# Performance work log

Hardware: AMD Instinct MI355X
Metric: run time of the kernel (lower is better)

Reference implementation:

```python
import jax, jax.numpy as jnp
import numpy as np

HEADS = 16
DMODEL = 1024
DPH = DMODEL // HEADS  # 64
MAX_REL = 32
B, S = 4, 1024


def setup_inputs() -> dict:
    key = jax.random.key(0)
    ks = jax.random.split(key, 16)
    f = lambda k, shape: jax.random.normal(k, shape, dtype=jnp.float32)
    scale = 1.0 / np.sqrt(DMODEL)
    inp = {
        'key':   f(ks[0], (B, S, DMODEL)),
        'value': f(ks[1], (B, S, DMODEL)),
        'query': f(ks[2], (B, S, DMODEL)),
        'mask':  jax.random.randint(ks[3], (B, 1, S), 0, 2).astype(jnp.bool_),
        'Wq': f(ks[4], (DMODEL, DMODEL)) * scale,
        'bq': jnp.zeros((DMODEL,), jnp.float32),
        'Wk': f(ks[5], (DMODEL, DMODEL)) * scale,
        'bk': jnp.zeros((DMODEL,), jnp.float32),
        'Wv': f(ks[6], (DMODEL, DMODEL)) * scale,
        'bv': jnp.zeros((DMODEL,), jnp.float32),
        'Wo': f(ks[7], (DMODEL, DMODEL)) * scale,
        'bo': jnp.zeros((DMODEL,), jnp.float32),
        'rel_emb': f(ks[8], (2 * MAX_REL + 1, DPH)) * 0.02,
    }
    return inp


def _rel_pos_matrix(length, max_rel):
    r = jnp.arange(length)
    dist = r[None, :] - r[:, None]            # [S,S]
    return jnp.clip(dist, -max_rel, max_rel) + max_rel


def reference(key, value, query, mask, Wq, bq, Wk, bk, Wv, bv, Wo, bo, rel_emb):
    b, s, _ = query.shape
    # projections (no layer_cache, attn_type='self': q/k/v all from inputs)
    q = (query @ Wq + bq).reshape(b, s, HEADS, DPH).transpose(0, 2, 1, 3)  # [B,H,S,D]
    k = (key   @ Wk + bk).reshape(b, s, HEADS, DPH).transpose(0, 2, 1, 3)
    v = (value @ Wv + bv).reshape(b, s, HEADS, DPH).transpose(0, 2, 1, 3)

    # relative position embeddings (keys and values share the same table lookup)
    rel_idx = _rel_pos_matrix(s, MAX_REL)      # [S,S] int
    relations = rel_emb[rel_idx]               # [S,S,D]

    q = q / jnp.sqrt(jnp.asarray(DPH, q.dtype))
    scores = jnp.einsum('bhqd,bhkd->bhqk', q, k)
    scores = scores + jnp.einsum('bhqd,qkd->bhqk', q, relations)
    scores = jnp.where(mask[:, None, :, :], -1e18, scores)  # mask [B,1,1,S] broadcast
    attn = jax.nn.softmax(scores, axis=-1)
    # dropout p=0.0 (eval): identity
    ctx = jnp.einsum('bhqk,bhkd->bhqd', attn, v)
    ctx = ctx + jnp.einsum('bhqk,qkd->bhqd', attn, relations)
    ctx = ctx.transpose(0, 2, 1, 3).reshape(b, s, HEADS * DPH)
    out = ctx @ Wo + bo
    top_attn = attn[:, 0]
    return out, top_attn
```

## Files before the change

kernel.cpp:

```cpp
#include <hip/hip_runtime.h>

typedef unsigned short u16;
typedef unsigned int   u32;
typedef short bf8v  __attribute__((ext_vector_type(8)));
typedef short s16x4 __attribute__((ext_vector_type(4)));
typedef float f32x4 __attribute__((ext_vector_type(4)));

#define DEV static __device__ __forceinline__
#define MBYTE (1u<<20)

DEV u16 f2b(float f) {
    u32 u = __builtin_bit_cast(u32, f);
    u32 r = (u + 0x7fffu + ((u >> 16) & 1u)) >> 16;
    return (u16)r;
}
DEV float b2f(u16 s) { return __builtin_bit_cast(float, (u32)s << 16); }
DEV bf8v ld8(const u16* p) { return *reinterpret_cast<const bf8v*>(p); }

DEV bf8v ldelems(const void* X, long idx, int f32f) {
    if (f32f) {
        const float* p = (const float*)X + idx;
        f32x4 a = *(const f32x4*)p;
        f32x4 b = *(const f32x4*)(p + 4);
        bf8v r;
        r[0] = (short)f2b(a[0]); r[1] = (short)f2b(a[1]);
        r[2] = (short)f2b(a[2]); r[3] = (short)f2b(a[3]);
        r[4] = (short)f2b(b[0]); r[5] = (short)f2b(b[1]);
        r[6] = (short)f2b(b[2]); r[7] = (short)f2b(b[3]);
        return r;
    }
    return ld8((const u16*)X + idx);
}
DEV float ldscalar(const void* X, long idx, int f32f) {
    return f32f ? ((const float*)X)[idx] : b2f(((const u16*)X)[idx]);
}

DEV f32x4 mfma_(bf8v a, bf8v b, f32x4 c) {
    return __builtin_amdgcn_mfma_f32_16x16x32_bf16(a, b, c, 0, 0, 0);
}

DEV void gload16(void* lds, const void* g) {
    __builtin_amdgcn_global_load_lds(
        (const __attribute__((address_space(1))) void*)g,
        (__attribute__((address_space(3))) void*)lds,
        16, 0, 0);
}

__global__ __launch_bounds__(256) void sniffrelk(const u32* q, const u32* m,
                                                 const void* rel, u16* relT, int* flags) {
    __shared__ int c1s, c2s;
    int t = threadIdx.x;
    if (t == 0) { c1s = 0; c2s = 0; }
    __syncthreads();
    int c1 = 0, c2 = 0;
    for (int i = t; i < 1024; i += 256) {
        u32 u = q[i];
        int e = (int)((u >> 23) & 0xff);
        if (u == 0u || (e >= 118 && e <= 134)) c1++;
        if (m[i] > 1u) c2++;
    }
    atomicAdd(&c1s, c1);
    atomicAdd(&c2s, c2);
    __syncthreads();
    int f32f = (c1s > 512) ? 1 : 0;
    if (t == 0) { flags[0] = f32f; flags[1] = (c2s > 100) ? 1 : 0; }
    for (int i = t; i < 64 * 64; i += 256) {
        int d = i >> 6, r = i & 63;
        relT[i] = f32f ? f2b(((const float*)rel)[r * 64 + d]) : ((const u16*)rel)[r * 64 + d];
    }
}

__global__ __launch_bounds__(256) void tposek(const void* s0, const void* s1,
                                              const void* s2, const void* s3,
                                              u16* d0, u16* d1, u16* d2, u16* d3,
                                              const int* flags) {
    __shared__ u16 tile[64][65];
    int f32f = flags[0];
    int z = blockIdx.z;
    const void* src = z == 0 ? s0 : (z == 1 ? s1 : (z == 2 ? s2 : s3));
    u16*       dst = z == 0 ? d0 : (z == 1 ? d1 : (z == 2 ? d2 : d3));
    int t = threadIdx.x;
    int r0 = blockIdx.y * 64, c0 = blockIdx.x * 64;
#pragma unroll
    for (int i = 0; i < 16; ++i) {
        int u = i * 256 + t;
        int row = u >> 6, col = u & 63;
        long gi = (long)(r0 + row) * 1024 + c0 + col;
        tile[row][col] = f32f ? f2b(((const float*)src)[gi]) : ((const u16*)src)[gi];
    }
    __syncthreads();
#pragma unroll
    for (int i = 0; i < 8; ++i) {
        int u = i * 256 + t;
        int row = u >> 5, col = (u & 31) * 2;
        u32 v = (u32)tile[col][row] | ((u32)tile[col + 1][row] << 16);
        *(u32*)(dst + (long)(c0 + row) * 1024 + r0 + col) = v;
    }
}

__global__ __launch_bounds__(512) void gemm128(
    const void* x0, const void* x1, const void* x2,
    const u16* w0, const u16* w1, const u16* w2,
    const void* b0, const void* b1, const void* b2,
    void* c0, void* c1, void* c2, int mode_base,
    const int* flags, int a_use_flag) {
    __shared__ __align__(16) u16 Al[128 * 32];
    __shared__ __align__(16) u16 Bl[128 * 32];

    int j = blockIdx.x;
    int nwg = gridDim.x;
    int ppx = nwg >> 6;
    int xcd = j & 7, idx = j >> 3;
    int panel = xcd * ppx + (idx >> 3);
    int n0 = (idx & 7) * 128;
    int m0 = (panel & 31) * 128;
    int z  = panel >> 5;

    const void* X    = z == 0 ? x0 : (z == 1 ? x1 : x2);
    const u16*  BT   = z == 0 ? w0 : (z == 1 ? w1 : w2);
    const void* bias = z == 0 ? b0 : (z == 1 ? b1 : b2);
    void*       C    = z == 0 ? c0 : (z == 1 ? c1 : c2);
    int mode = mode_base + z;
    int f32m = flags[0];
    int f32a = a_use_flag ? f32m : 0;

    int t = threadIdx.x, w = t >> 6, l = t & 63;
    int lr = l & 15, lg = l >> 4;
    int wr = (w >> 1) * 32, wc = (w & 1) * 64;

    int rS = t >> 2;
    int sP = t & 3;
    int sL = sP ^ ((rS >> 1) & 3);

    f32x4 acc[2][4];
    f32x4 zf = {0.f, 0.f, 0.f, 0.f};
#pragma unroll
    for (int mt = 0; mt < 2; ++mt)
#pragma unroll
        for (int nt = 0; nt < 4; ++nt) acc[mt][nt] = zf;

    for (int kk = 0; kk < 32; ++kk) {
        __syncthreads();
        gload16((char*)Bl + w * 1024,
                (const char*)BT + (long)(n0 + rS) * 2048 + (long)kk * 64 + sL * 16);
        bf8v va = ldelems(X, (long)(m0 + rS) * 1024 + kk * 32 + sL * 8, f32a);
        *(bf8v*)((char*)Al + rS * 64 + sP * 16) = va;
        __syncthreads();
        bf8v af[2], bfr[4];
#pragma unroll
        for (int mt = 0; mt < 2; ++mt) {
            int r = wr + mt * 16 + lr;
            af[mt] = *(const bf8v*)((const char*)Al + r * 64 + ((lg * 16) ^ (((r >> 1) & 3) << 4)));
        }
#pragma unroll
        for (int nt = 0; nt < 4; ++nt) {
            int r = wc + nt * 16 + lr;
            bfr[nt] = *(const bf8v*)((const char*)Bl + r * 64 + ((lg * 16) ^ (((r >> 1) & 3) << 4)));
        }
#pragma unroll
        for (int mt = 0; mt < 2; ++mt)
#pragma unroll
            for (int nt = 0; nt < 4; ++nt) acc[mt][nt] = mfma_(af[mt], bfr[nt], acc[mt][nt]);
    }

#pragma unroll
    for (int nt = 0; nt < 4; ++nt) {
        int col = n0 + wc + nt * 16 + lr;
        float bv = f32m ? ((const float*)bias)[col] : b2f(((const u16*)bias)[col]);
#pragma unroll
        for (int mt = 0; mt < 2; ++mt) {
#pragma unroll
            for (int r = 0; r < 4; ++r) {
                int m = m0 + wr + mt * 16 + lg * 4 + r;
                float v = acc[mt][nt][r] + bv;
                if (mode == 0) v *= 0.125f;
                if (mode <= 1) {
                    int bb = m >> 10, s = m & 1023, hh = col >> 6, dd = col & 63;
                    ((u16*)C)[(((bb << 4) + hh) * 1024 + s) * 64 + dd] = f2b(v);
                } else if (mode == 2) {
                    int bb = m >> 10, s = m & 1023, hh = col >> 6, dd = col & 63;
                    ((u16*)C)[(((bb << 4) + hh) * 64 + dd) * 1024 + s] = f2b(v);
                } else {
                    long idx2 = (long)m * 1024 + col;
                    if (f32m) ((float*)C)[idx2] = v; else ((u16*)C)[idx2] = f2b(v);
                }
            }
        }
    }
}

__global__ __launch_bounds__(256) void attnk(
    const u16* __restrict__ Qw, const u16* __restrict__ Kw, const u16* __restrict__ Vtw,
    const void* __restrict__ rel, const u16* __restrict__ relT,
    const void* __restrict__ mask,
    u16* __restrict__ ctx, void* __restrict__ dout, u16* __restrict__ linv_g,
    const int* __restrict__ flags) {
    __shared__ __align__(16) u16 Klds[2][32 * 64];
    __shared__ __align__(16) u16 Vlds[2][64 * 32];
    __shared__ u16 qrelB[64][64];
    __shared__ __align__(16) u16 P_lds[4][16][40];
    __shared__ __align__(16) u16 arel_lds[4][16][64];
    __shared__ float linv_lds[64];
    __shared__ float tlo_lds[64], thi_lds[64];
    __shared__ u16 maskB[1024];

    int f32f = flags[0], m8 = flags[1];
    float* attnF = (float*)dout + 4194304;
    u16*   attnB = (u16*)dout + 4194304;

    int t = threadIdx.x, w = t >> 6, l = t & 63;
    int lr = l & 15, lg = l >> 4;
    int id = blockIdx.x;
    int xcd = id & 7, j = id >> 3;
    int bh = xcd * 8 + (j & 7);
    int qb = j >> 3;
    int b = bh >> 4, h = bh & 15;
    int q0 = qb * 64;
    int qw0 = q0 + w * 16;
    const u16* Qh  = Qw  + (((b << 4) + h) << 16);
    const u16* Kh  = Kw  + (((b << 4) + h) << 16);
    const u16* Vth = Vtw + (((b << 4) + h) << 16);

    int rowK = w * 8 + (l >> 3);
    int scK  = 16 * ((l & 7) ^ ((l >> 3) & 7));
    int rowV = w * 16 + (l >> 2);
    int scV  = ((l & 3) * 16) ^ (((l >> 2) & 3) << 4);
    gload16((char*)&Klds[0][0] + w * 1024, (const char*)Kh + (long)rowK * 128 + scK);
    gload16((char*)&Vlds[0][0] + w * 1024, (const char*)Vth + (long)rowV * 2048 + scV);

    for (int i = t; i < 1024; i += 256) {
        int mv = m8 ? (int)((const unsigned char*)mask)[(b << 10) + i]
                    : ((const int*)mask)[(b << 10) + i];
        maskB[i] = mv ? f2b(-1.0e18f) : 0;
    }
#pragma unroll
    for (int i = 0; i < 8; ++i) ((u32*)&arel_lds[0][0][0])[t + i * 256] = 0;

    int qg = q0 + w * 16 + lr;
    bf8v qf0 = ld8(Qh + qg * 64 + lg * 8);
    bf8v qf1 = ld8(Qh + qg * 64 + 32 + lg * 8);

    float lo_src = 0.f, hi_src = 0.f;
#pragma unroll
    for (int rt = 0; rt < 5; ++rt) {
        int rrow = rt * 16 + lr; if (rrow > 64) rrow = 64;
        f32x4 aq = {0.f, 0.f, 0.f, 0.f};
        aq = mfma_(ldelems(rel, rrow * 64 + lg * 8, f32f), qf0, aq);
        aq = mfma_(ldelems(rel, rrow * 64 + 32 + lg * 8, f32f), qf1, aq);
        if (rt < 4) {
#pragma unroll
            for (int r = 0; r < 4; ++r) qrelB[w * 16 + lr][rt * 16 + lg * 4 + r] = f2b(aq[r]);
            if (rt == 0) lo_src = aq[0];
        } else {
            hi_src = aq[0];
        }
    }
    float qrel_lo = __shfl(lo_src, lr);
    float qrel_hi = __shfl(hi_src, lr);
    const u16* qrow_rel = qrelB[w * 16 + lr];

    __syncthreads();

    float l_run = 0.f, tlo = 0.f, thi = 0.f;
    f32x4 acc[4];
#pragma unroll
    for (int dt = 0; dt < 4; ++dt) acc[dt] = f32x4{0.f, 0.f, 0.f, 0.f};

    for (int kc = 0; kc < 32; ++kc) {
        int cur = kc & 1;
        int k0 = kc * 32;
        if (kc < 31) {
            int k1 = k0 + 32;
            gload16((char*)&Klds[cur ^ 1][0] + w * 1024,
                    (const char*)Kh + (long)(k1 + rowK) * 128 + scK);
            gload16((char*)&Vlds[cur ^ 1][0] + w * 1024,
                    (const char*)Vth + (long)rowV * 2048 + k1 * 2 + scV);
        }
        const char* KB = (const char*)&Klds[cur][0];
        const char* VB = (const char*)&Vlds[cur][0];

        bf8v kf0 = *(const bf8v*)(KB + lr * 128 + ((lg * 16) ^ ((lr & 7) << 4)));
        bf8v kf1 = *(const bf8v*)(KB + lr * 128 + ((64 + lg * 16) ^ ((lr & 7) << 4)));
        bf8v kf2 = *(const bf8v*)(KB + (16 + lr) * 128 + ((lg * 16) ^ ((lr & 7) << 4)));
        bf8v kf3 = *(const bf8v*)(KB + (16 + lr) * 128 + ((64 + lg * 16) ^ ((lr & 7) << 4)));
        f32x4 zf = {0.f, 0.f, 0.f, 0.f};
        f32x4 s0 = mfma_(kf0, qf0, zf); s0 = mfma_(kf1, qf1, s0);
        f32x4 s1 = mfma_(kf2, qf0, zf); s1 = mfma_(kf3, qf1, s1);

        int cls = (k0 + 63 < qw0) ? 0 : ((k0 > qw0 + 47) ? 1 : 2);
        f32x4 p0v, p1v;
#pragma unroll
        for (int r = 0; r < 4; ++r) {
            int key0 = k0 + lg * 4 + r, key1 = key0 + 16;
            float r0, r1;
            if (cls == 0)      { r0 = qrel_lo; r1 = qrel_lo; }
            else if (cls == 1) { r0 = qrel_hi; r1 = qrel_hi; }
            else {
                int d0 = key0 - qg, d1 = key1 - qg;
                r0 = (d0 <= -32) ? qrel_lo : ((d0 >= 32) ? qrel_hi : b2f(qrow_rel[d0 + 32]));
                r1 = (d1 <= -32) ? qrel_lo : ((d1 >= 32) ? qrel_hi : b2f(qrow_rel[d1 + 32]));
            }
            p0v[r] = __expf(s0[r] + r0 + b2f(maskB[key0]));
            p1v[r] = __expf(s1[r] + r1 + b2f(maskB[key1]));
            l_run += p0v[r] + p1v[r];
        }
        s16x4 pk0 = { (short)f2b(p0v[0]), (short)f2b(p0v[1]), (short)f2b(p0v[2]), (short)f2b(p0v[3]) };
        s16x4 pk1 = { (short)f2b(p1v[0]), (short)f2b(p1v[1]), (short)f2b(p1v[2]), (short)f2b(p1v[3]) };
        *(s16x4*)&P_lds[w][lr][lg * 4]      = pk0;
        *(s16x4*)&P_lds[w][lr][16 + lg * 4] = pk1;
        if (cls == 2) {
#pragma unroll
            for (int r = 0; r < 4; ++r) {
                int key0 = k0 + lg * 4 + r, key1 = key0 + 16;
                int d0 = key0 - qg, d1 = key1 - qg;
                if (d0 > -32 && d0 < 32) arel_lds[w][lr][d0 + 32] = (u16)pk0[r];
                else if (d0 <= -32) tlo += p0v[r]; else thi += p0v[r];
                if (d1 > -32 && d1 < 32) arel_lds[w][lr][d1 + 32] = (u16)pk1[r];
                else if (d1 <= -32) tlo += p1v[r]; else thi += p1v[r];
            }
        } else {
            float s8 = (p0v[0] + p0v[1] + p0v[2] + p0v[3]) + (p1v[0] + p1v[1] + p1v[2] + p1v[3]);
            if (cls == 0) tlo += s8; else thi += s8;
        }
        if (h == 0) {
            long a0 = (long)((b << 10) + qg) * 1024 + k0 + lg * 4;
            if (f32f) {
                *(f32x4*)(attnF + a0) = p0v;
                *(f32x4*)(attnF + a0 + 16) = p1v;
            } else {
                *(s16x4*)(attnB + a0) = pk0;
                *(s16x4*)(attnB + a0 + 16) = pk1;
            }
        }
        __builtin_amdgcn_sched_barrier(0);
        bf8v pa = ld8(&P_lds[w][lr][lg * 8]);
#pragma unroll
        for (int dt = 0; dt < 4; ++dt) {
            bf8v vb = *(const bf8v*)(VB + (dt * 16 + lr) * 64 + ((lg * 16) ^ ((lr & 3) << 4)));
            acc[dt] = mfma_(pa, vb, acc[dt]);
        }
        __syncthreads();
    }

    l_run += __shfl_xor(l_run, 16); l_run += __shfl_xor(l_run, 32);
    tlo   += __shfl_xor(tlo, 16);   tlo   += __shfl_xor(tlo, 32);
    thi   += __shfl_xor(thi, 16);   thi   += __shfl_xor(thi, 32);
    float inv_l = 1.0f / l_run;
    if (lg == 0) {
        linv_lds[w * 16 + lr] = inv_l;
        tlo_lds[w * 16 + lr] = tlo;
        thi_lds[w * 16 + lr] = thi;
        if (h == 0) linv_g[(b << 10) + qg] = f2b(inv_l);
    }

#pragma unroll
    for (int ks = 0; ks < 2; ++ks) {
        bf8v aa = ld8(&arel_lds[w][lr][ks * 32 + lg * 8]);
#pragma unroll
        for (int dt = 0; dt < 4; ++dt) {
            bf8v rb = ld8(relT + (dt * 16 + lr) * 64 + ks * 32 + lg * 8);
            acc[dt] = mfma_(aa, rb, acc[dt]);
        }
    }

    float r0v[4], r64v[4];
#pragma unroll
    for (int dt = 0; dt < 4; ++dt) {
        int d = dt * 16 + lr;
        r0v[dt]  = ldscalar(rel, d, f32f);
        r64v[dt] = ldscalar(rel, 64 * 64 + d, f32f);
    }

#pragma unroll
    for (int dt = 0; dt < 4; ++dt) {
#pragma unroll
        for (int r = 0; r < 4; ++r) {
            int qrow = w * 16 + lg * 4 + r;
            float v = (acc[dt][r] + tlo_lds[qrow] * r0v[dt] + thi_lds[qrow] * r64v[dt])
                      * linv_lds[qrow];
            int qgr = q0 + qrow;
            ctx[((b << 10) + qgr) * 1024 + (h << 6) + dt * 16 + lr] = f2b(v);
        }
    }
}

__global__ __launch_bounds__(256) void rescalek(void* dout, const u16* linv_g,
                                                const int* flags) {
    int f32f = flags[0];
    long gid = (long)blockIdx.x * 256 + threadIdx.x;
    long e0 = gid * 8;
    float inv = b2f(linv_g[e0 >> 10]);
    if (f32f) {
        float* a = (float*)dout + 4194304 + e0;
        f32x4 v0 = *(f32x4*)a, v1 = *(f32x4*)(a + 4);
#pragma unroll
        for (int r = 0; r < 4; ++r) { v0[r] *= inv; v1[r] *= inv; }
        *(f32x4*)a = v0; *(f32x4*)(a + 4) = v1;
    } else {
        u16* a = (u16*)dout + 4194304 + e0;
        bf8v v = *(bf8v*)a;
        bf8v o;
#pragma unroll
        for (int r = 0; r < 8; ++r) o[r] = (short)f2b(b2f((u16)v[r]) * inv);
        *(bf8v*)a = o;
    }
}

extern "C" void kernel_launch(void* const* d_in, const int* in_sizes, int n_in,
                              void* d_out, int out_size, void* d_ws, size_t ws_size,
                              hipStream_t stream) {
    const void* key   = d_in[0];
    const void* value = d_in[1];
    const void* query = d_in[2];
    const void* mask  = d_in[3];
    const void* Wq = d_in[4];  const void* bq = d_in[5];
    const void* Wk = d_in[6];  const void* bk = d_in[7];
    const void* Wv = d_in[8];  const void* bv = d_in[9];
    const void* Wo = d_in[10]; const void* bo = d_in[11];
    const void* rel = d_in[12];

    char* ws = (char*)d_ws;
    u16* WqT  = (u16*)(ws + 0 * MBYTE);
    u16* WkT  = (u16*)(ws + 2 * MBYTE);
    u16* WvT  = (u16*)(ws + 4 * MBYTE);
    u16* WoT  = (u16*)(ws + 6 * MBYTE);
    u16* Qws  = (u16*)(ws + 8 * MBYTE);
    u16* Kws  = (u16*)(ws + 16 * MBYTE);
    u16* Vtws = (u16*)(ws + 24 * MBYTE);
    u16* ctxw = (u16*)(ws + 32 * MBYTE);
    int* flags = (int*)(ws + 40 * MBYTE);
    u16* linv_g = (u16*)(ws + 40 * MBYTE + 16);

    u16* relT = (u16*)d_out;

    sniffrelk<<<dim3(1), 256, 0, stream>>>((const u32*)query, (const u32*)mask, rel, relT, flags);
    tposek<<<dim3(16, 16, 4), 256, 0, stream>>>(Wq, Wk, Wv, Wo, WqT, WkT, WvT, WoT, flags);
    gemm128<<<dim3(768), 512, 0, stream>>>(query, key, value, WqT, WkT, WvT,
                                           bq, bk, bv, Qws, Kws, Vtws, 0, flags, 1);
    attnk<<<dim3(1024), 256, 0, stream>>>(Qws, Kws, Vtws, rel, relT, mask,
                                          ctxw, d_out, linv_g, flags);
    rescalek<<<dim3(2048), 256, 0, stream>>>(d_out, linv_g, flags);
    gemm128<<<dim3(256), 512, 0, stream>>>(ctxw, ctxw, ctxw, WoT, WoT, WoT,
                                           bo, bo, bo, d_out, d_out, d_out, 3, flags, 0);
}
```

Measured before the change: 180.3 us.

## Double-buffer GEMM LDS tiles and fold attention rescale into attention kernel

The GEMM main loop now uses two LDS buffers, so the next K-slice is fetched while MFMAs run on the current one, and each iteration needs one barrier instead of two. The separate rescale kernel is removed. The h==0 attention blocks now multiply their own rows of the top-head attention output by 1/l after the context write, which saves a launch and the global round trip of linv. The cost is double the GEMM LDS footprint, which may reduce occupancy. The h==0 blocks also carry extra tail work, which could leave the grid unbalanced.

```diff
diff --git a/kernel.cpp b/kernel.cpp
--- a/kernel.cpp
+++ b/kernel.cpp
@@ -104,8 +104,8 @@
     const void* b0, const void* b1, const void* b2,
     void* c0, void* c1, void* c2, int mode_base,
     const int* flags, int a_use_flag) {
-    __shared__ __align__(16) u16 Al[128 * 32];
-    __shared__ __align__(16) u16 Bl[128 * 32];
+    __shared__ __align__(16) u16 Al[2][128 * 32];
+    __shared__ __align__(16) u16 Bl[2][128 * 32];
 
     int j = blockIdx.x;
     int nwg = gridDim.x;
@@ -139,28 +139,39 @@
 #pragma unroll
         for (int nt = 0; nt < 4; ++nt) acc[mt][nt] = zf;
 
+    gload16((char*)Bl[0] + w * 1024,
+            (const char*)BT + (long)(n0 + rS) * 2048 + sL * 16);
+    bf8v va0 = ldelems(X, (long)(m0 + rS) * 1024 + sL * 8, f32a);
+    *(bf8v*)((char*)Al[0] + rS * 64 + sP * 16) = va0;
+    __syncthreads();
+
+    int cur = 0;
     for (int kk = 0; kk < 32; ++kk) {
-        __syncthreads();
-        gload16((char*)Bl + w * 1024,
-                (const char*)BT + (long)(n0 + rS) * 2048 + (long)kk * 64 + sL * 16);
-        bf8v va = ldelems(X, (long)(m0 + rS) * 1024 + kk * 32 + sL * 8, f32a);
-        *(bf8v*)((char*)Al + rS * 64 + sP * 16) = va;
-        __syncthreads();
+        int nxt = cur ^ 1;
+        bf8v va_n;
+        if (kk < 31) {
+            gload16((char*)Bl[nxt] + w * 1024,
+                    (const char*)BT + (long)(n0 + rS) * 2048 + (long)(kk + 1) * 64 + sL * 16);
+            va_n = ldelems(X, (long)(m0 + rS) * 1024 + (kk + 1) * 32 + sL * 8, f32a);
+        }
         bf8v af[2], bfr[4];
 #pragma unroll
         for (int mt = 0; mt < 2; ++mt) {
             int r = wr + mt * 16 + lr;
-            af[mt] = *(const bf8v*)((const char*)Al + r * 64 + ((lg * 16) ^ (((r >> 1) & 3) << 4)));
+            af[mt] = *(const bf8v*)((const char*)Al[cur] + r * 64 + ((lg * 16) ^ (((r >> 1) & 3) << 4)));
         }
 #pragma unroll
         for (int nt = 0; nt < 4; ++nt) {
             int r = wc + nt * 16 + lr;
-            bfr[nt] = *(const bf8v*)((const char*)Bl + r * 64 + ((lg * 16) ^ (((r >> 1) & 3) << 4)));
+            bfr[nt] = *(const bf8v*)((const char*)Bl[cur] + r * 64 + ((lg * 16) ^ (((r >> 1) & 3) << 4)));
         }
 #pragma unroll
         for (int mt = 0; mt < 2; ++mt)
 #pragma unroll
             for (int nt = 0; nt < 4; ++nt) acc[mt][nt] = mfma_(af[mt], bfr[nt], acc[mt][nt]);
+        if (kk < 31) *(bf8v*)((char*)Al[nxt] + rS * 64 + sP * 16) = va_n;
+        __syncthreads();
+        cur = nxt;
     }
 
 #pragma unroll
@@ -193,7 +204,7 @@
     const u16* __restrict__ Qw, const u16* __restrict__ Kw, const u16* __restrict__ Vtw,
     const void* __restrict__ rel, const u16* __restrict__ relT,
     const void* __restrict__ mask,
-    u16* __restrict__ ctx, void* __restrict__ dout, u16* __restrict__ linv_g,
+    u16* __restrict__ ctx, void* __restrict__ dout,
     const int* __restrict__ flags) {
     __shared__ __align__(16) u16 Klds[2][32 * 64];
     __shared__ __align__(16) u16 Vlds[2][64 * 32];
@@ -350,7 +361,6 @@
         linv_lds[w * 16 + lr] = inv_l;
         tlo_lds[w * 16 + lr] = tlo;
         thi_lds[w * 16 + lr] = thi;
-        if (h == 0) linv_g[(b << 10) + qg] = f2b(inv_l);
     }
 
 #pragma unroll
@@ -382,27 +392,28 @@
             ctx[((b << 10) + qgr) * 1024 + (h << 6) + dt * 16 + lr] = f2b(v);
         }
     }
-}
-
-__global__ __launch_bounds__(256) void rescalek(void* dout, const u16* linv_g,
-                                                const int* flags) {
-    int f32f = flags[0];
-    long gid = (long)blockIdx.x * 256 + threadIdx.x;
-    long e0 = gid * 8;
-    float inv = b2f(linv_g[e0 >> 10]);
-    if (f32f) {
-        float* a = (float*)dout + 4194304 + e0;
-        f32x4 v0 = *(f32x4*)a, v1 = *(f32x4*)(a + 4);
-#pragma unroll
-        for (int r = 0; r < 4; ++r) { v0[r] *= inv; v1[r] *= inv; }
-        *(f32x4*)a = v0; *(f32x4*)(a + 4) = v1;
-    } else {
-        u16* a = (u16*)dout + 4194304 + e0;
-        bf8v v = *(bf8v*)a;
-        bf8v o;
-#pragma unroll
-        for (int r = 0; r < 8; ++r) o[r] = (short)f2b(b2f((u16)v[r]) * inv);
-        *(bf8v*)a = o;
+
+    if (h == 0) {
+        __syncthreads();
+        for (int i = t; i < 64 * 128; i += 256) {
+            int row = i >> 7, ch = i & 127;
+            float inv = linv_lds[row];
+            long base = (long)((b << 10) + q0 + row) * 1024 + ch * 8;
+            if (f32f) {
+                f32x4 v0 = *(f32x4*)(attnF + base);
+                f32x4 v1 = *(f32x4*)(attnF + base + 4);
+#pragma unroll
+                for (int r = 0; r < 4; ++r) { v0[r] *= inv; v1[r] *= inv; }
+                *(f32x4*)(attnF + base) = v0;
+                *(f32x4*)(attnF + base + 4) = v1;
+            } else {
+                bf8v v = *(bf8v*)(attnB + base);
+                bf8v o;
+#pragma unroll
+                for (int r = 0; r < 8; ++r) o[r] = (short)f2b(b2f((u16)v[r]) * inv);
+                *(bf8v*)(attnB + base) = o;
+            }
+        }
     }
 }
 
@@ -429,7 +440,6 @@
     u16* Vtws = (u16*)(ws + 24 * MBYTE);
     u16* ctxw = (u16*)(ws + 32 * MBYTE);
     int* flags = (int*)(ws + 40 * MBYTE);
-    u16* linv_g = (u16*)(ws + 40 * MBYTE + 16);
 
     u16* relT = (u16*)d_out;
 
@@ -438,8 +448,7 @@
     gemm128<<<dim3(768), 512, 0, stream>>>(query, key, value, WqT, WkT, WvT,
                                            bq, bk, bv, Qws, Kws, Vtws, 0, flags, 1);
     attnk<<<dim3(1024), 256, 0, stream>>>(Qws, Kws, Vtws, rel, relT, mask,
-                                          ctxw, d_out, linv_g, flags);
-    rescalek<<<dim3(2048), 256, 0, stream>>>(d_out, linv_g, flags);
+                                          ctxw, d_out, flags);
     gemm128<<<dim3(256), 512, 0, stream>>>(ctxw, ctxw, ctxw, WoT, WoT, WoT,
                                            bo, bo, bo, d_out, d_out, d_out, 3, flags, 0);
 }
```

After: 197.5 us. 9.5% more time.

## Double-buffer GEMM LDS tiles with K=64 steps and prefetch next tile

Applied to the files above, without the earlier changes.

Reworks the projection GEMM main loop to use two LDS buffers with a K-step of 64 instead of 32. The next tile's global loads are issued before the MFMAs on the current tile, and there is one barrier per iteration instead of two. The intent is to hide global-load latency and cut synchronisation overhead. In exchange, LDS use grows to 64KB per block, which may lower occupancy, and the register-staged A loads raise register pressure.

```diff
diff --git a/kernel.cpp b/kernel.cpp
--- a/kernel.cpp
+++ b/kernel.cpp
@@ -104,8 +104,8 @@
     const void* b0, const void* b1, const void* b2,
     void* c0, void* c1, void* c2, int mode_base,
     const int* flags, int a_use_flag) {
-    __shared__ __align__(16) u16 Al[128 * 32];
-    __shared__ __align__(16) u16 Bl[128 * 32];
+    __shared__ __align__(16) u16 Al[2][128 * 64];
+    __shared__ __align__(16) u16 Bl[2][128 * 64];
 
     int j = blockIdx.x;
     int nwg = gridDim.x;
@@ -128,9 +128,8 @@
     int lr = l & 15, lg = l >> 4;
     int wr = (w >> 1) * 32, wc = (w & 1) * 64;
 
-    int rS = t >> 2;
-    int sP = t & 3;
-    int sL = sP ^ ((rS >> 1) & 3);
+    int rowS = w * 8 + (l >> 3);
+    int sLt  = (l & 7) ^ ((l >> 3) & 7);
 
     f32x4 acc[2][4];
     f32x4 zf = {0.f, 0.f, 0.f, 0.f};
@@ -139,28 +138,55 @@
 #pragma unroll
         for (int nt = 0; nt < 4; ++nt) acc[mt][nt] = zf;
 
-    for (int kk = 0; kk < 32; ++kk) {
+#pragma unroll
+    for (int c = 0; c < 2; ++c) {
+        int row = c * 64 + rowS;
+        gload16((char*)Bl[0] + c * 8192 + w * 1024,
+                (const char*)BT + (long)(n0 + row) * 2048 + sLt * 16);
+        bf8v va = ldelems(X, (long)(m0 + row) * 1024 + sLt * 8, f32a);
+        *(bf8v*)((char*)Al[0] + (c * 512 + t) * 16) = va;
+    }
+    __syncthreads();
+
+    int cur = 0;
+    for (int kk = 0; kk < 16; ++kk) {
+        int nxt = cur ^ 1;
+        bf8v vaA, vaB;
+        if (kk < 15) {
+            int row0 = 0 * 64 + rowS, row1 = 1 * 64 + rowS;
+            gload16((char*)Bl[nxt] + 0 * 8192 + w * 1024,
+                    (const char*)BT + (long)(n0 + row0) * 2048 + (long)(kk + 1) * 128 + sLt * 16);
+            gload16((char*)Bl[nxt] + 1 * 8192 + w * 1024,
+                    (const char*)BT + (long)(n0 + row1) * 2048 + (long)(kk + 1) * 128 + sLt * 16);
+            vaA = ldelems(X, (long)(m0 + row0) * 1024 + (kk + 1) * 64 + sLt * 8, f32a);
+            vaB = ldelems(X, (long)(m0 + row1) * 1024 + (kk + 1) * 64 + sLt * 8, f32a);
+        }
+#pragma unroll
+        for (int ks = 0; ks < 2; ++ks) {
+            bf8v af[2], bfr[4];
+#pragma unroll
+            for (int mt = 0; mt < 2; ++mt) {
+                int r = wr + mt * 16 + lr;
+                af[mt] = *(const bf8v*)((const char*)Al[cur] + r * 128
+                                        + 16 * ((ks * 4 + lg) ^ (r & 7)));
+            }
+#pragma unroll
+            for (int nt = 0; nt < 4; ++nt) {
+                int r = wc + nt * 16 + lr;
+                bfr[nt] = *(const bf8v*)((const char*)Bl[cur] + r * 128
+                                         + 16 * ((ks * 4 + lg) ^ (r & 7)));
+            }
+#pragma unroll
+            for (int mt = 0; mt < 2; ++mt)
+#pragma unroll
+                for (int nt = 0; nt < 4; ++nt) acc[mt][nt] = mfma_(af[mt], bfr[nt], acc[mt][nt]);
+        }
+        if (kk < 15) {
+            *(bf8v*)((char*)Al[nxt] + (0 * 512 + t) * 16) = vaA;
+            *(bf8v*)((char*)Al[nxt] + (1 * 512 + t) * 16) = vaB;
+        }
         __syncthreads();
-        gload16((char*)Bl + w * 1024,
-                (const char*)BT + (long)(n0 + rS) * 2048 + (long)kk * 64 + sL * 16);
-        bf8v va = ldelems(X, (long)(m0 + rS) * 1024 + kk * 32 + sL * 8, f32a);
-        *(bf8v*)((char*)Al + rS * 64 + sP * 16) = va;
-        __syncthreads();
-        bf8v af[2], bfr[4];
-#pragma unroll
-        for (int mt = 0; mt < 2; ++mt) {
-            int r = wr + mt * 16 + lr;
-            af[mt] = *(const bf8v*)((const char*)Al + r * 64 + ((lg * 16) ^ (((r >> 1) & 3) << 4)));
-        }
-#pragma unroll
-        for (int nt = 0; nt < 4; ++nt) {
-            int r = wc + nt * 16 + lr;
-            bfr[nt] = *(const bf8v*)((const char*)Bl + r * 64 + ((lg * 16) ^ (((r >> 1) & 3) << 4)));
-        }
-#pragma unroll
-        for (int mt = 0; mt < 2; ++mt)
-#pragma unroll
-            for (int nt = 0; nt < 4; ++nt) acc[mt][nt] = mfma_(af[mt], bfr[nt], acc[mt][nt]);
+        cur = nxt;
     }
 
 #pragma unroll
```

Result: slower. 188.4 us (+4.5%).
